# Optimization experiments

Measured on AMD Instinct MI355X. Metric: run time of the kernel, lower is better.

Reference implementation:

```python
import jax, jax.numpy as jnp
import numpy as np

EMBED_DIMS = [8, 16, 8]      # prod = 1024 = embed_dim
HIDDEN_DIMS = [16, 16, 16]   # prod = 4096 = hidden_dim
RANK = 16
B, S = 4, 1024


def _make_cores(key, in_dims, out_dims, rank):
    d = len(in_dims)
    ranks = [1] + [rank] * (d - 1) + [1]
    cores = []
    for k in range(d):
        key, sub = jax.random.split(key)
        shape = (ranks[k], in_dims[k], out_dims[k], ranks[k + 1])
        scale = 1.0 / np.sqrt(in_dims[k] * ranks[k])
        cores.append((scale * jax.random.normal(sub, shape, dtype=jnp.float32)))
    return cores


def setup_inputs() -> dict:
    key = jax.random.key(0)
    k_x, k1, k2, kb1, kb2 = jax.random.split(key, 5)
    x = jax.random.normal(k_x, (B, S, 1024), dtype=jnp.float32)
    fc1 = _make_cores(k1, EMBED_DIMS, HIDDEN_DIMS, RANK)
    fc2 = _make_cores(k2, HIDDEN_DIMS, EMBED_DIMS, RANK)
    b1 = 0.01 * jax.random.normal(kb1, (4096,), dtype=jnp.float32)
    b2 = 0.01 * jax.random.normal(kb2, (1024,), dtype=jnp.float32)
    return {
        "x": x,
        "fc1_c0": fc1[0], "fc1_c1": fc1[1], "fc1_c2": fc1[2], "fc1_b": b1,
        "fc2_c0": fc2[0], "fc2_c1": fc2[1], "fc2_c2": fc2[2], "fc2_b": b2,
    }


def tt_linear(x_flat, cores, bias, in_dims):
    """TT-matrix x batch-of-vectors product. x_flat: [N, prod(in_dims)].

    Cores: core_k has shape [r_{k-1}, n_k, m_k, r_k] with r_0 = r_d = 1.
    Invariant: acc is [r_{k-1}, n_k, rest] with rest laid out as
    (n_{k+1}..n_d, N, m_1..m_{k-1}).
    """
    N = x_flat.shape[0]
    acc = x_flat.reshape((N,) + tuple(in_dims))      # [N, n1..nd]
    acc = jnp.moveaxis(acc, 0, -1)                   # [n1..nd, N]
    acc = acc.reshape(in_dims[0], -1)[None]          # [1, n1, rest]
    d = len(cores)
    for k, c in enumerate(cores):
        # contract previous rank + current input mode
        acc = jnp.einsum('pnR,pnmq->Rmq', acc, c)    # [rest, m_k, r_k]
        if k < d - 1:
            n_next = in_dims[k + 1]
            R, m, q = acc.shape
            acc = acc.reshape(n_next, R // n_next, m, q)
            acc = jnp.transpose(acc, (3, 0, 1, 2)).reshape(q, n_next, -1)
    # final acc: [N * m1..m_{d-1}, m_d, 1] -> [N, M]
    return acc.reshape(N, -1) + bias


def reference(x, fc1_c0, fc1_c1, fc1_c2, fc1_b, fc2_c0, fc2_c1, fc2_c2, fc2_b):
    flat = x.reshape(-1, x.shape[-1])                        # [N, embed_dim]
    z1 = tt_linear(flat, [fc1_c0, fc1_c1, fc1_c2], fc1_b, EMBED_DIMS)   # [N, hidden]
    h1 = jax.nn.gelu(z1, approximate=False)                  # exact erf GELU (torch default)
    z2 = tt_linear(h1, [fc2_c0, fc2_c1, fc2_c2], fc2_b, HIDDEN_DIMS)    # [N, embed]
    return z2.reshape(*x.shape[:-1], z2.shape[-1])
```

## Files before the change

### kernel.cpp

```cpp
#include <hip/hip_runtime.h>
#include <stdint.h>

__device__ __forceinline__ float b2f(unsigned short u) {
    union { uint32_t i; float f; } v; v.i = ((uint32_t)u) << 16; return v.f;
}
__device__ __forceinline__ unsigned short f2b(float f) {
    union { float f; uint32_t i; } v; v.f = f;
    uint32_t r = v.i + 0x7fffu + ((v.i >> 16) & 1u);
    return (unsigned short)(r >> 16);
}

typedef __bf16 bf16x8 __attribute__((ext_vector_type(8)));
typedef float  f32x16 __attribute__((ext_vector_type(16)));

__global__ __launch_bounds__(256)
void cvt_f32_bf16(const float* __restrict__ x, unsigned short* __restrict__ xb) {
    int t = blockIdx.x * 256 + threadIdx.x;
    const float4* p = (const float4*)(x + (size_t)t * 8);
    float4 f0 = p[0], f1 = p[1];
    int4 o;
    o.x = (uint32_t)f2b(f0.x) | ((uint32_t)f2b(f0.y) << 16);
    o.y = (uint32_t)f2b(f0.z) | ((uint32_t)f2b(f0.w) << 16);
    o.z = (uint32_t)f2b(f1.x) | ((uint32_t)f2b(f1.y) << 16);
    o.w = (uint32_t)f2b(f1.z) | ((uint32_t)f2b(f1.w) << 16);
    ((int4*)xb)[t] = o;
}

template<int N3, int M3>
__global__ void build_T(const float* __restrict__ c1,
                        const float* __restrict__ c2,
                        float* __restrict__ T) {
    int e = blockIdx.x * 256 + threadIdx.x;
    int m3 = e % M3;
    int t  = e / M3;
    int n3 = t % N3;
    int rm = t / N3;
    float s = 0.f;
#pragma unroll
    for (int r2 = 0; r2 < 16; ++r2)
        s += c1[rm * 16 + r2] * c2[(r2 * N3 + n3) * M3 + m3];
    T[e] = s;
}

template<int N1, int N2, int N3, int M1, int M2, int M3>
__global__ __launch_bounds__(256)
void build_W(const float* __restrict__ c0,
             const float* __restrict__ T,
             unsigned short* __restrict__ W) {
    constexpr int K = N1 * N2 * N3;
    int t  = blockIdx.x * 256 + threadIdx.x;
    int m3 = t % M3;
    int m2 = (t / M3) % M2;
    int n2 = (t / (M3 * M2)) % N2;
    int m1 = (t / (M3 * M2 * N2)) % M1;
    int n1 =  t / (M3 * M2 * N2 * M1);

    float c0r[16];
    const float4* c0p = (const float4*)(c0 + (n1 * M1 + m1) * 16);
#pragma unroll
    for (int i = 0; i < 4; ++i) ((float4*)c0r)[i] = c0p[i];

    float acc[N3] = {};
#pragma unroll
    for (int r1 = 0; r1 < 16; ++r1) {
        const float* Tp = T + (size_t)(((r1 * 16 + n2) * 16 + m2) * N3) * M3 + m3;
#pragma unroll
        for (int n3 = 0; n3 < N3; ++n3)
            acc[n3] += c0r[r1] * Tp[n3 * M3];
    }

    unsigned short ob[N3];
#pragma unroll
    for (int n3 = 0; n3 < N3; ++n3) ob[n3] = f2b(acc[n3]);

    unsigned short* dst = W + (size_t)((m1 * M2 + m2) * M3 + m3) * K
                            + (n1 * N2 + n2) * N3;
#pragma unroll
    for (int c = 0; c < N3 / 8; ++c)
        ((int4*)dst)[c] = ((const int4*)ob)[c];
}

template<int BM, int BN, int NSUB, int KTOT, bool DO_GELU, bool A_F32, bool C_F32>
__global__ __launch_bounds__(256, 2)
void gemm32v2(const void* __restrict__ Av,
              const unsigned short* __restrict__ Bt,
              const float* __restrict__ bias,
              void* __restrict__ Cv,
              int Ncols) {
    constexpr int FI  = BM / 64;
    constexpr int FJ  = BN / 64;
    constexpr int ASZ = BM * 64;
    constexpr int BSZ = BN * 64;
    constexpr int PA  = BM / 32;
    constexpr int PB  = BN / 32;
    __shared__ unsigned short As[NSUB * ASZ];
    __shared__ unsigned short Bs[NSUB * BSZ];

    const int tid  = threadIdx.x;
    const int lane = tid & 63;
    const int wave = tid >> 6;
    const int rowBase = blockIdx.y * BM;
    const int colBase = blockIdx.x * BN;

    const int waveM = (wave >> 1) * (BM / 2);
    const int waveN = (wave & 1) * (BN / 2);

    f32x16 acc[FI][FJ] = {};

    const int lr    = lane >> 3;
    const int jj    = lane & 7;
    const int m32   = lane & 31;
    const int khalf = lane >> 5;

    for (int k0 = 0; k0 < KTOT; k0 += NSUB * 64) {
#pragma unroll
        for (int s = 0; s < NSUB; ++s) {
            const int kk = k0 + s * 64;
#pragma unroll
            for (int it = 0; it < PA; ++it) {
                const int c  = wave * PA + it;
                const int jg = jj ^ lr ^ (c & 7);
                const size_t aoff = (size_t)(rowBase + c * 8 + lr) * KTOT + kk + jg * 8;
                int4 v;
                if (A_F32) {
                    const float* ga = (const float*)Av + aoff;
                    float4 f0 = *(const float4*)ga;
                    float4 f1 = *(const float4*)(ga + 4);
                    v.x = (uint32_t)f2b(f0.x) | ((uint32_t)f2b(f0.y) << 16);
                    v.y = (uint32_t)f2b(f0.z) | ((uint32_t)f2b(f0.w) << 16);
                    v.z = (uint32_t)f2b(f1.x) | ((uint32_t)f2b(f1.y) << 16);
                    v.w = (uint32_t)f2b(f1.z) | ((uint32_t)f2b(f1.w) << 16);
                } else {
                    v = *(const int4*)((const unsigned short*)Av + aoff);
                }
                *(int4*)&As[s * ASZ + c * 512 + lane * 8] = v;
            }
#pragma unroll
            for (int it = 0; it < PB; ++it) {
                const int c  = wave * PB + it;
                const int jg = jj ^ lr ^ (c & 7);
                *(int4*)&Bs[s * BSZ + c * 512 + lane * 8] =
                    *(const int4*)(Bt + (size_t)(colBase + c * 8 + lr) * KTOT + kk + jg * 8);
            }
        }
        __syncthreads();

#pragma unroll
        for (int s = 0; s < NSUB; ++s) {
#pragma unroll
            for (int ks = 0; ks < 4; ++ks) {
                bf16x8 a_f[FI], b_f[FJ];
#pragma unroll
                for (int i = 0; i < FI; ++i) {
                    const int key  = (m32 & 7) ^
                        ((((waveM >> 3) + 4 * i) + (m32 >> 3)) & 7);
                    const int slot = ((ks * 2 + khalf) ^ key) * 8;
                    a_f[i] = *(const bf16x8*)&As[s * ASZ +
                              (waveM + i * 32 + m32) * 64 + slot];
                }
#pragma unroll
                for (int j = 0; j < FJ; ++j) {
                    const int key  = (m32 & 7) ^
                        ((((waveN >> 3) + 4 * j) + (m32 >> 3)) & 7);
                    const int slot = ((ks * 2 + khalf) ^ key) * 8;
                    b_f[j] = *(const bf16x8*)&Bs[s * BSZ +
                              (waveN + j * 32 + m32) * 64 + slot];
                }
#pragma unroll
                for (int i = 0; i < FI; ++i)
#pragma unroll
                    for (int j = 0; j < FJ; ++j)
                        acc[i][j] = __builtin_amdgcn_mfma_f32_32x32x16_bf16(
                            a_f[i], b_f[j], acc[i][j], 0, 0, 0);
            }
        }
        __syncthreads();
    }

#pragma unroll
    for (int i = 0; i < FI; ++i) {
#pragma unroll
        for (int j = 0; j < FJ; ++j) {
            const int col = colBase + waveN + j * 32 + m32;
            const float bv = bias[col];
#pragma unroll
            for (int reg = 0; reg < 16; ++reg) {
                const int row = rowBase + waveM + i * 32 +
                                (reg & 3) + 8 * (reg >> 2) + 4 * khalf;
                float z = acc[i][j][reg] + bv;
                if (DO_GELU)
                    z = 0.5f * z * (1.f + erff(z * 0.70710678118654752f));
                const size_t off = (size_t)row * Ncols + col;
                if (C_F32) ((float*)Cv)[off] = z;
                else       ((unsigned short*)Cv)[off] = f2b(z);
            }
        }
    }
}

extern "C" void kernel_launch(void* const* d_in, const int* in_sizes, int n_in,
                              void* d_out, int out_size, void* d_ws, size_t ws_size,
                              hipStream_t stream) {
    const float* x      = (const float*)d_in[0];
    const float* fc1_c0 = (const float*)d_in[1];
    const float* fc1_c1 = (const float*)d_in[2];
    const float* fc1_c2 = (const float*)d_in[3];
    const float* fc1_b  = (const float*)d_in[4];
    const float* fc2_c0 = (const float*)d_in[5];
    const float* fc2_c1 = (const float*)d_in[6];
    const float* fc2_c2 = (const float*)d_in[7];
    const float* fc2_b  = (const float*)d_in[8];

    char* ws = (char*)d_ws;
    unsigned short* W  = (unsigned short*)(ws);
    float*          T  = (float*)(ws + (8u << 20));
    const bool big = ws_size >= (50ull << 20);
    unsigned short* xb = (unsigned short*)(ws + (10u << 20));
    unsigned short* h  = (unsigned short*)(ws + (big ? (18u << 20) : (10u << 20)));

    build_T<8, 16><<<2048, 256, 0, stream>>>(fc1_c1, fc1_c2, T);
    build_W<8, 16, 8, 16, 16, 16><<<2048, 256, 0, stream>>>(fc1_c0, T, W);
    if (big) {
        cvt_f32_bf16<<<2048, 256, 0, stream>>>(x, xb);
        gemm32v2<256, 128, 1, 1024, true, false, false>
            <<<dim3(32, 16), 256, 0, stream>>>(xb, W, fc1_b, h, 4096);
    } else {
        gemm32v2<256, 128, 1, 1024, true, true, false>
            <<<dim3(32, 16), 256, 0, stream>>>(x, W, fc1_b, h, 4096);
    }

    build_T<16, 8><<<2048, 256, 0, stream>>>(fc2_c1, fc2_c2, T);
    build_W<16, 16, 16, 8, 16, 8><<<1024, 256, 0, stream>>>(fc2_c0, T, W);
    gemm32v2<64, 128, 2, 4096, false, false, true>
        <<<dim3(8, 64), 256, 0, stream>>>(h, W, fc2_b, d_out, 1024);
}
```

Before: 229.0 us.

## Fuse TT-core weight construction for both layers into one prep kernel

Replaces the separate build_T and build_W launches for each layer with a single prep kernel. Each block computes its slice of the intermediate core product in shared memory and then writes dense bf16 weights, and one launch builds both layers' weights when the workspace is large enough. It also drops the separate f32-to-bf16 conversion of x and lets the first GEMM convert while loading. The goal is fewer launches and no global round trip for the intermediate, at the cost of redoing the fp32 conversion inside the GEMM's A-tile loads.

```diff
diff --git a/kernel.cpp b/kernel.cpp
--- a/kernel.cpp
+++ b/kernel.cpp
@@ -13,71 +13,78 @@
 typedef __bf16 bf16x8 __attribute__((ext_vector_type(8)));
 typedef float  f32x16 __attribute__((ext_vector_type(16)));
 
+template<int N1, int N2, int N3, int M1, int M2, int M3>
+__device__ __forceinline__ void build_layer(int b, int tid,
+                                            const float* __restrict__ c0,
+                                            const float* __restrict__ c1,
+                                            const float* __restrict__ c2,
+                                            unsigned short* __restrict__ W,
+                                            float* Ts) {
+    constexpr int K = N1 * N2 * N3;
+    const int n2 = b / M2;
+    const int m2 = b % M2;
+
+#pragma unroll
+    for (int e = 0; e < 8; ++e) {
+        const int idx = e * 256 + tid;
+        const int m3 = idx % M3;
+        const int n3 = (idx / M3) % N3;
+        const int r1 = idx / (M3 * N3);
+        float s = 0.f;
+#pragma unroll
+        for (int r2 = 0; r2 < 16; ++r2)
+            s += c1[((r1 * N2 + n2) * M2 + m2) * 16 + r2] *
+                 c2[(r2 * N3 + n3) * M3 + m3];
+        Ts[idx] = s;
+    }
+    __syncthreads();
+
+    constexpr int C   = M1 * M3;
+    constexpr int P   = 256 / C;
+    constexpr int NCH = N1 / P;
+    const int combo  = tid % C;
+    const int m1     = combo / M3;
+    const int m3     = combo % M3;
+    const int n1base = (tid / C) * NCH;
+
+#pragma unroll
+    for (int ni = 0; ni < NCH; ++ni) {
+        const int n1 = n1base + ni;
+        float acc[N3] = {};
+#pragma unroll
+        for (int r1 = 0; r1 < 16; ++r1) {
+            const float c0v = c0[(n1 * M1 + m1) * 16 + r1];
+#pragma unroll
+            for (int n3 = 0; n3 < N3; ++n3)
+                acc[n3] += c0v * Ts[(r1 * N3 + n3) * M3 + m3];
+        }
+        unsigned short ob[N3];
+#pragma unroll
+        for (int n3 = 0; n3 < N3; ++n3) ob[n3] = f2b(acc[n3]);
+        unsigned short* dst = W + (size_t)((m1 * M2 + m2) * M3 + m3) * K
+                                + (n1 * N2 + n2) * N3;
+#pragma unroll
+        for (int c = 0; c < N3 / 8; ++c)
+            ((int4*)dst)[c] = ((const int4*)ob)[c];
+    }
+}
+
+template<int WHICH>
 __global__ __launch_bounds__(256)
-void cvt_f32_bf16(const float* __restrict__ x, unsigned short* __restrict__ xb) {
-    int t = blockIdx.x * 256 + threadIdx.x;
-    const float4* p = (const float4*)(x + (size_t)t * 8);
-    float4 f0 = p[0], f1 = p[1];
-    int4 o;
-    o.x = (uint32_t)f2b(f0.x) | ((uint32_t)f2b(f0.y) << 16);
-    o.y = (uint32_t)f2b(f0.z) | ((uint32_t)f2b(f0.w) << 16);
-    o.z = (uint32_t)f2b(f1.x) | ((uint32_t)f2b(f1.y) << 16);
-    o.w = (uint32_t)f2b(f1.z) | ((uint32_t)f2b(f1.w) << 16);
-    ((int4*)xb)[t] = o;
-}
-
-template<int N3, int M3>
-__global__ void build_T(const float* __restrict__ c1,
-                        const float* __restrict__ c2,
-                        float* __restrict__ T) {
-    int e = blockIdx.x * 256 + threadIdx.x;
-    int m3 = e % M3;
-    int t  = e / M3;
-    int n3 = t % N3;
-    int rm = t / N3;
-    float s = 0.f;
-#pragma unroll
-    for (int r2 = 0; r2 < 16; ++r2)
-        s += c1[rm * 16 + r2] * c2[(r2 * N3 + n3) * M3 + m3];
-    T[e] = s;
-}
-
-template<int N1, int N2, int N3, int M1, int M2, int M3>
-__global__ __launch_bounds__(256)
-void build_W(const float* __restrict__ c0,
-             const float* __restrict__ T,
-             unsigned short* __restrict__ W) {
-    constexpr int K = N1 * N2 * N3;
-    int t  = blockIdx.x * 256 + threadIdx.x;
-    int m3 = t % M3;
-    int m2 = (t / M3) % M2;
-    int n2 = (t / (M3 * M2)) % N2;
-    int m1 = (t / (M3 * M2 * N2)) % M1;
-    int n1 =  t / (M3 * M2 * N2 * M1);
-
-    float c0r[16];
-    const float4* c0p = (const float4*)(c0 + (n1 * M1 + m1) * 16);
-#pragma unroll
-    for (int i = 0; i < 4; ++i) ((float4*)c0r)[i] = c0p[i];
-
-    float acc[N3] = {};
-#pragma unroll
-    for (int r1 = 0; r1 < 16; ++r1) {
-        const float* Tp = T + (size_t)(((r1 * 16 + n2) * 16 + m2) * N3) * M3 + m3;
-#pragma unroll
-        for (int n3 = 0; n3 < N3; ++n3)
-            acc[n3] += c0r[r1] * Tp[n3 * M3];
-    }
-
-    unsigned short ob[N3];
-#pragma unroll
-    for (int n3 = 0; n3 < N3; ++n3) ob[n3] = f2b(acc[n3]);
-
-    unsigned short* dst = W + (size_t)((m1 * M2 + m2) * M3 + m3) * K
-                            + (n1 * N2 + n2) * N3;
-#pragma unroll
-    for (int c = 0; c < N3 / 8; ++c)
-        ((int4*)dst)[c] = ((const int4*)ob)[c];
+void prep(const float* __restrict__ f1c0, const float* __restrict__ f1c1,
+          const float* __restrict__ f1c2,
+          const float* __restrict__ f2c0, const float* __restrict__ f2c1,
+          const float* __restrict__ f2c2,
+          unsigned short* __restrict__ W1, unsigned short* __restrict__ W2) {
+    __shared__ float Ts[2048];
+    const int tid = threadIdx.x;
+    if (WHICH == 1 || (WHICH == 0 && blockIdx.x < 256)) {
+        build_layer<8, 16, 8, 16, 16, 16>(blockIdx.x & 255, tid,
+                                          f1c0, f1c1, f1c2, W1, Ts);
+    } else {
+        build_layer<16, 16, 16, 8, 16, 8>(blockIdx.x & 255, tid,
+                                          f2c0, f2c1, f2c2, W2, Ts);
+    }
 }
 
 template<int BM, int BN, int NSUB, int KTOT, bool DO_GELU, bool A_F32, bool C_F32>
@@ -212,25 +219,30 @@
     const float* fc2_b  = (const float*)d_in[8];
 
     char* ws = (char*)d_ws;
-    unsigned short* W  = (unsigned short*)(ws);
-    float*          T  = (float*)(ws + (8u << 20));
-    const bool big = ws_size >= (50ull << 20);
-    unsigned short* xb = (unsigned short*)(ws + (10u << 20));
-    unsigned short* h  = (unsigned short*)(ws + (big ? (18u << 20) : (10u << 20)));
-
-    build_T<8, 16><<<2048, 256, 0, stream>>>(fc1_c1, fc1_c2, T);
-    build_W<8, 16, 8, 16, 16, 16><<<2048, 256, 0, stream>>>(fc1_c0, T, W);
+    const bool big = ws_size >= (48ull << 20);
+
     if (big) {
-        cvt_f32_bf16<<<2048, 256, 0, stream>>>(x, xb);
-        gemm32v2<256, 128, 1, 1024, true, false, false>
-            <<<dim3(32, 16), 256, 0, stream>>>(xb, W, fc1_b, h, 4096);
+        unsigned short* W1 = (unsigned short*)(ws);
+        unsigned short* W2 = (unsigned short*)(ws + (8u << 20));
+        unsigned short* h  = (unsigned short*)(ws + (16u << 20));
+
+        prep<0><<<512, 256, 0, stream>>>(fc1_c0, fc1_c1, fc1_c2,
+                                         fc2_c0, fc2_c1, fc2_c2, W1, W2);
+        gemm32v2<256, 128, 1, 1024, true, true, false>
+            <<<dim3(32, 16), 256, 0, stream>>>(x, W1, fc1_b, h, 4096);
+        gemm32v2<64, 128, 2, 4096, false, false, true>
+            <<<dim3(8, 64), 256, 0, stream>>>(h, W2, fc2_b, d_out, 1024);
     } else {
+        unsigned short* W = (unsigned short*)(ws);
+        unsigned short* h = (unsigned short*)(ws + (8u << 20));
+
+        prep<1><<<256, 256, 0, stream>>>(fc1_c0, fc1_c1, fc1_c2,
+                                         fc2_c0, fc2_c1, fc2_c2, W, W);
         gemm32v2<256, 128, 1, 1024, true, true, false>
             <<<dim3(32, 16), 256, 0, stream>>>(x, W, fc1_b, h, 4096);
-    }
-
-    build_T<16, 8><<<2048, 256, 0, stream>>>(fc2_c1, fc2_c2, T);
-    build_W<16, 16, 16, 8, 16, 8><<<1024, 256, 0, stream>>>(fc2_c0, T, W);
-    gemm32v2<64, 128, 2, 4096, false, false, true>
-        <<<dim3(8, 64), 256, 0, stream>>>(h, W, fc2_b, d_out, 1024);
-}
+        prep<2><<<256, 256, 0, stream>>>(fc1_c0, fc1_c1, fc1_c2,
+                                         fc2_c0, fc2_c1, fc2_c2, W, W);
+        gemm32v2<64, 128, 2, 4096, false, false, true>
+            <<<dim3(8, 64), 256, 0, stream>>>(h, W, fc2_b, d_out, 1024);
+    }
+}
```

Result: slower. 366.5 us (+60.0%).
